# Optimization experiments

Measured on AMD Instinct MI355X. Metric: run time of the kernel, lower is better.

Reference implementation:

```python
import jax, jax.numpy as jnp
import numpy as np

B = 4096      # number of graphs (segments)
D = 256       # node feature dim
N = B * 64    # total nodes across the batch


def setup_inputs() -> dict:
    key = jax.random.key(0)
    x = jax.random.normal(key, (N, D), dtype=jnp.float32)
    # ragged per-graph node counts: strictly positive, sum exactly to N
    rng = np.random.default_rng(0)
    sizes = 1 + rng.multinomial(N - B, np.full(B, 1.0 / B))
    feature_size_list = jnp.asarray(sizes, dtype=jnp.int64)
    return {"x": x, "feature_size_list": feature_size_list}


def reference(x, feature_size_list):
    # Fused segment-mean: one pass over x instead of a Python loop with cat.
    num_segments = feature_size_list.shape[0]  # static
    seg_ids = jnp.repeat(
        jnp.arange(num_segments), feature_size_list, total_repeat_length=x.shape[0]
    )
    sums = jax.ops.segment_sum(x, seg_ids, num_segments=num_segments)  # [B, D]
    return sums / feature_size_list[:, None].astype(x.dtype)
```

## Files before the change

### kernel.cpp

```cpp
#include <hip/hip_runtime.h>


#define NSEG 4096

typedef float f32x4 __attribute__((ext_vector_type(4)));

__global__ __launch_bounds__(256) void seg_mean_fused_kernel(
    const float* __restrict__ x,
    const int* __restrict__ sizes,
    float* __restrict__ out) {
    const int b   = blockIdx.x;
    const int tid = threadIdx.x;
    const int tx  = tid & 63;
    const int ty  = tid >> 6;

    int partial = 0;
    for (int i = tid; i < b; i += 256) partial += sizes[i];
#pragma unroll
    for (int off = 32; off > 0; off >>= 1)
        partial += __shfl_down(partial, off, 64);

    __shared__ int swave[4];
    __shared__ int s_start;
    if (tx == 0) swave[ty] = partial;
    __syncthreads();
    if (tid == 0) s_start = swave[0] + swave[1] + swave[2] + swave[3];
    __syncthreads();

    const int size     = sizes[b];
    const size_t start = (size_t)s_start;

    const f32x4* xr = reinterpret_cast<const f32x4*>(x) + start * 64 + tx;

    f32x4 a0 = {0.f, 0.f, 0.f, 0.f};
    f32x4 a1 = {0.f, 0.f, 0.f, 0.f};
    f32x4 a2 = {0.f, 0.f, 0.f, 0.f};
    f32x4 a3 = {0.f, 0.f, 0.f, 0.f};

    int r = ty;
    for (; r + 16 <= size; r += 16) {
        f32x4 v0 = __builtin_nontemporal_load(&xr[(size_t)r * 64]);
        f32x4 v1 = __builtin_nontemporal_load(&xr[(size_t)(r + 4) * 64]);
        f32x4 v2 = __builtin_nontemporal_load(&xr[(size_t)(r + 8) * 64]);
        f32x4 v3 = __builtin_nontemporal_load(&xr[(size_t)(r + 12) * 64]);
        a0 += v0;
        a1 += v1;
        a2 += v2;
        a3 += v3;
    }
    for (; r < size; r += 4) {
        f32x4 v0 = __builtin_nontemporal_load(&xr[(size_t)r * 64]);
        a0 += v0;
    }
    a0 += a1;
    a2 += a3;
    a0 += a2;

    __shared__ f32x4 sh[256];
    sh[tid] = a0;
    __syncthreads();

    if (ty == 0) {
        f32x4 s = sh[tx] + sh[tx + 64] + sh[tx + 128] + sh[tx + 192];
        float fs = (float)size;
        f32x4 o = s / fs;
        __builtin_nontemporal_store(o, &reinterpret_cast<f32x4*>(out)[(size_t)b * 64 + tx]);
    }
}

extern "C" void kernel_launch(void* const* d_in, const int* in_sizes, int n_in,
                              void* d_out, int out_size, void* d_ws, size_t ws_size,
                              hipStream_t stream) {
    const float* x = (const float*)d_in[0];
    const int* sizes = (const int*)d_in[1];
    float* out = (float*)d_out;

    seg_mean_fused_kernel<<<NSEG, 256, 0, stream>>>(x, sizes, out);
}
```

Baseline: 48.41 us.

## Assign one wavefront per segment and pack four segments per block

Each 256-thread block now handles four consecutive segments, one per wavefront, instead of one segment split across four wavefronts. This removes the cross-wave shared-memory reduction and one barrier. The prefix sum over earlier sizes is read as int4 vectors, which quarters the block count and the redundant prefix work. The cost is less parallelism inside each segment and possible imbalance between waves in a block, since segment sizes differ.

```diff
diff --git a/kernel.cpp b/kernel.cpp
--- a/kernel.cpp
+++ b/kernel.cpp
@@ -4,68 +4,72 @@
 #define NSEG 4096
 
 typedef float f32x4 __attribute__((ext_vector_type(4)));
+typedef int   i32x4 __attribute__((ext_vector_type(4)));
 
-__global__ __launch_bounds__(256) void seg_mean_fused_kernel(
+__global__ __launch_bounds__(256) void seg_mean_wave_kernel(
     const float* __restrict__ x,
     const int* __restrict__ sizes,
     float* __restrict__ out) {
     const int b   = blockIdx.x;
     const int tid = threadIdx.x;
     const int tx  = tid & 63;
-    const int ty  = tid >> 6;
+    const int w   = tid >> 6;
+    const int g0  = b * 4;
 
+    const i32x4* s4 = reinterpret_cast<const i32x4*>(sizes);
     int partial = 0;
-    for (int i = tid; i < b; i += 256) partial += sizes[i];
+#pragma unroll
+    for (int k = 0; k < 4; ++k) {
+        int c = tid + k * 256;
+        if (c < b) {
+            i32x4 v = s4[c];
+            partial += v.x + v.y + v.z + v.w;
+        }
+    }
 #pragma unroll
     for (int off = 32; off > 0; off >>= 1)
         partial += __shfl_down(partial, off, 64);
 
     __shared__ int swave[4];
-    __shared__ int s_start;
-    if (tx == 0) swave[ty] = partial;
+    if (tx == 0) swave[w] = partial;
     __syncthreads();
-    if (tid == 0) s_start = swave[0] + swave[1] + swave[2] + swave[3];
-    __syncthreads();
+    const int base = swave[0] + swave[1] + swave[2] + swave[3];
 
-    const int size     = sizes[b];
-    const size_t start = (size_t)s_start;
+    i32x4 ls = s4[b];
+    int off = base;
+    if (w > 0) off += ls.x;
+    if (w > 1) off += ls.y;
+    if (w > 2) off += ls.z;
+    const int sz = (w == 0) ? ls.x : (w == 1) ? ls.y : (w == 2) ? ls.z : ls.w;
+    const int seg = g0 + w;
 
-    const f32x4* xr = reinterpret_cast<const f32x4*>(x) + start * 64 + tx;
+    const f32x4* p = reinterpret_cast<const f32x4*>(x) + (size_t)off * 64 + tx;
 
     f32x4 a0 = {0.f, 0.f, 0.f, 0.f};
     f32x4 a1 = {0.f, 0.f, 0.f, 0.f};
     f32x4 a2 = {0.f, 0.f, 0.f, 0.f};
     f32x4 a3 = {0.f, 0.f, 0.f, 0.f};
 
-    int r = ty;
-    for (; r + 16 <= size; r += 16) {
-        f32x4 v0 = __builtin_nontemporal_load(&xr[(size_t)r * 64]);
-        f32x4 v1 = __builtin_nontemporal_load(&xr[(size_t)(r + 4) * 64]);
-        f32x4 v2 = __builtin_nontemporal_load(&xr[(size_t)(r + 8) * 64]);
-        f32x4 v3 = __builtin_nontemporal_load(&xr[(size_t)(r + 12) * 64]);
+    int r = 0;
+    for (; r + 4 <= sz; r += 4) {
+        f32x4 v0 = __builtin_nontemporal_load(&p[(r + 0) * 64]);
+        f32x4 v1 = __builtin_nontemporal_load(&p[(r + 1) * 64]);
+        f32x4 v2 = __builtin_nontemporal_load(&p[(r + 2) * 64]);
+        f32x4 v3 = __builtin_nontemporal_load(&p[(r + 3) * 64]);
         a0 += v0;
         a1 += v1;
         a2 += v2;
         a3 += v3;
     }
-    for (; r < size; r += 4) {
-        f32x4 v0 = __builtin_nontemporal_load(&xr[(size_t)r * 64]);
-        a0 += v0;
-    }
+    for (; r < sz; ++r)
+        a0 += __builtin_nontemporal_load(&p[r * 64]);
+
     a0 += a1;
     a2 += a3;
     a0 += a2;
 
-    __shared__ f32x4 sh[256];
-    sh[tid] = a0;
-    __syncthreads();
-
-    if (ty == 0) {
-        f32x4 s = sh[tx] + sh[tx + 64] + sh[tx + 128] + sh[tx + 192];
-        float fs = (float)size;
-        f32x4 o = s / fs;
-        __builtin_nontemporal_store(o, &reinterpret_cast<f32x4*>(out)[(size_t)b * 64 + tx]);
-    }
+    f32x4 o = a0 / (float)sz;
+    __builtin_nontemporal_store(o, &reinterpret_cast<f32x4*>(out)[(size_t)seg * 64 + tx]);
 }
 
 extern "C" void kernel_launch(void* const* d_in, const int* in_sizes, int n_in,
@@ -75,5 +79,5 @@
     const int* sizes = (const int*)d_in[1];
     float* out = (float*)d_out;
 
-    seg_mean_fused_kernel<<<NSEG, 256, 0, stream>>>(x, sizes, out);
+    seg_mean_wave_kernel<<<NSEG / 4, 256, 0, stream>>>(x, sizes, out);
 }
```

After: 47.71 us. No clear change (-1.5%).
